# Kernel tuning notes

Hardware: AMD Instinct MI355X
Metric: run time of the kernel (lower is better)

## Reference

```python
import jax, jax.numpy as jnp
import numpy as np

V_K = 1.0
SIGMA = 0.1
EPS = 1e-10


def setup_inputs() -> dict:
    key = jax.random.key(0)
    ks = jax.random.split(key, 5)
    M, L, N, d, H = 2, 6, 512, 2, 64
    data = jax.random.normal(ks[0], (M, L, N, d), dtype=jnp.float32)
    t_snapshots = jnp.arange(L, dtype=jnp.float32) * 0.1
    w1 = jax.random.normal(ks[1], (H,), dtype=jnp.float32) * 0.5
    b1 = jnp.zeros((H,), jnp.float32)
    W2 = jax.random.normal(ks[2], (H, H), dtype=jnp.float32) / np.float32(np.sqrt(H))
    b2 = jnp.zeros((H,), jnp.float32)
    w3 = jax.random.normal(ks[3], (H,), dtype=jnp.float32) / np.float32(np.sqrt(H))
    b3 = jnp.zeros((), jnp.float32)
    return {"data": data, "t_snapshots": t_snapshots, "w1": w1, "b1": b1,
            "W2": W2, "b2": b2, "w3": w3, "b3": b3}


def _phi(r, w1, b1, W2, b2, w3, b3):
    # scalar-to-scalar tanh MLP applied elementwise to r (any shape)
    h1 = jnp.tanh(r[..., None] * w1 + b1)                      # [..., H]
    h2 = jnp.tanh(jnp.einsum('...h,hk->...k', h1, W2) + b2)    # [..., H]
    return jnp.einsum('...k,k->...', h2, w3) + b3              # [...]


def _loss(data, t, params):
    M, L, N, d = data.shape
    diff = data[:, :, :, None, :] - data[:, :, None, :, :]     # [M,L,N,N,d]
    ssq = jnp.sum(diff * diff, axis=-1)                        # [M,L,N,N]
    dist = jnp.where(ssq > 0, jnp.sqrt(jnp.where(ssq > 0, ssq, 1.0)), 0.0)
    off_diag = ~jnp.eye(N, dtype=bool)                         # [N,N]

    f = lambda r: _phi(r, *params)
    # Phi values on all L snapshots (for energy)
    phi = f(dist)                                              # [M,L,N,N]
    # First/second radial derivatives on current snapshots only (ell = 0..L-2)
    r_cur = dist[:, :-1]                                       # [M,L-1,N,N]
    df = lambda r: jax.jvp(f, (r,), (jnp.ones_like(r),))[1]
    dphi = df(r_cur)                                           # Phi'(r)
    d2phi = jax.jvp(df, (r_cur,), (jnp.ones_like(r_cur),))[1]  # Phi''(r)

    dt = t[1:] - t[:-1]                                        # [L-1]

    # --- drift / dissipation ---
    dist_safe = jnp.maximum(r_cur, EPS)
    unit = diff[:, :-1] / dist_safe[..., None]                 # [M,L-1,N,N,d]
    gphi = jnp.where(off_diag[..., None], dphi[..., None] * unit, 0.0)
    grad_Phi_mean = gphi.sum(axis=3) / N                       # [M,L-1,N,d]
    drift = -V_K * data[:, :-1] - grad_Phi_mean
    total_diss = ((drift ** 2).sum(axis=(2, 3)) / N * dt).sum()

    # --- laplacian / diffusion ---
    lap_phi_mean = jnp.where(off_diag, d2phi, 0.0).sum(axis=-1) / N  # [M,L-1,N]
    lap_sum = V_K * d + lap_phi_mean
    total_diff = (SIGMA ** 2 * lap_sum.mean(axis=-1) * dt).sum()

    # --- energy per snapshot ---
    V_mean = 0.5 * V_K * (data ** 2).sum(axis=-1).mean(axis=-1)      # [M,L]
    Phi_mean = jnp.where(off_diag, phi, 0.0).sum(axis=(-1, -2)) / (N * N)
    E = V_mean + Phi_mean                                            # [M,L]
    total_energy_change = (E[:, 1:] - E[:, :-1]).sum()

    n_pairs = M * (L - 1)
    residual = (total_diss + total_diff - 2.0 * total_energy_change) / n_pairs
    return residual ** 2


def reference(data, t_snapshots, w1, b1, W2, b2, w3, b3):
    return _loss(data, t_snapshots, (w1, b1, W2, b2, w3, b3))
```

## Files before the change

kernel.cpp:

```cpp
#include <hip/hip_runtime.h>
#include <hip/hip_bf16.h>

#define MM 2
#define LL 6
#define NN 512
#define HH 64
#define K_TAB 512
#define RMAX 16.0f
#define H_STEP (RMAX / (float)K_TAB)
#define HINV   ((float)K_TAB / RMAX)
#define NBLK (MM * LL * (NN / 4))


__device__ __forceinline__ float wave_reduce_sum(float v) {
    #pragma unroll
    for (int m = 32; m > 0; m >>= 1) v += __shfl_xor(v, m, 64);
    return v;
}

__global__ __launch_bounds__(256) void build_nodes(
        const float* __restrict__ w1, const float* __restrict__ b1,
        const float* __restrict__ W2, const float* __restrict__ b2,
        const float* __restrict__ w3, const float* __restrict__ b3,
        float2* __restrict__ nodes) {
    int gid  = blockIdx.x * blockDim.x + threadIdx.x;
    int node = gid >> 6;
    int lane = gid & 63;
    if (node > K_TAB) return;

    float r = (float)node * H_STEP;

    float w1l = w1[lane];
    float u   = fmaf(r, w1l, b1[lane]);
    float t1  = tanhf(u);
    float e1  = 1.0f - t1 * t1;
    float h1  = t1;
    float h1p = e1 * w1l;

    float v = b2[lane], vp = 0.0f;
    #pragma unroll
    for (int h = 0; h < HH; ++h) {
        float a  = __shfl(h1,  h, 64);
        float ap = __shfl(h1p, h, 64);
        float w  = W2[h * HH + lane];
        v  = fmaf(a,  w, v);
        vp = fmaf(ap, w, vp);
    }
    float t2 = tanhf(v);
    float e2 = 1.0f - t2 * t2;
    float w3l = w3[lane];
    float sphi = wave_reduce_sum(w3l * t2);
    float sdp  = wave_reduce_sum(w3l * e2 * vp);
    if (lane == 0)
        nodes[node] = make_float2(sphi + b3[0], sdp * H_STEP);
}

__global__ __launch_bounds__(256) void pair_kernel(
        const float* __restrict__ data, const float2* __restrict__ nodes,
        float4* __restrict__ partial) {
    const int blocks_per_ml = NN / 4;
    int ml = blockIdx.x / blocks_per_ml;
    int i4 = blockIdx.x % blocks_per_ml;

    __shared__ float4 coef[K_TAB];
    __shared__ float2 xs[NN];
    __shared__ float  red[4 * 4];

    #pragma unroll
    for (int it = 0; it < K_TAB / 256; ++it) {
        int e = it * 256 + threadIdx.x;
        float2 g0 = nodes[e];
        float2 g1 = nodes[e + 1];
        float  d  = g1.x - g0.x;
        coef[e] = make_float4(g0.x, g0.y,
                              3.0f * d - 2.0f * g0.y - g1.y,
                              g0.y + g1.y - 2.0f * d);
    }
    {
        const float4* src = (const float4*)(data + (size_t)ml * NN * 2);
        ((float4*)xs)[threadIdx.x] = src[threadIdx.x];
    }
    __syncthreads();

    int wv   = threadIdx.x >> 6;
    int lane = threadIdx.x & 63;
    int i    = i4 * 4 + wv;
    float2 xi = xs[i];

    float aphi = 0.0f, ad2 = 0.0f, agx = 0.0f, agy = 0.0f;
    #pragma unroll
    for (int jj = 0; jj < NN / 64; ++jj) {
        int j = jj * 64 + lane;
        float2 xj = xs[j];
        float dx = xi.x - xj.x;
        float dy = xi.y - xj.y;
        float ssq = fmaf(dx, dx, dy * dy);
        float rr  = sqrtf(ssq);
        float f   = rr * HINV;
        int   idx = (int)f;
        idx = idx > (K_TAB - 1) ? (K_TAB - 1) : idx;
        float tt = f - (float)idx;
        float4 c = coef[idx];
        float phi  = fmaf(tt, fmaf(tt, fmaf(tt, c.w, c.z), c.y), c.x);
        float dph  = fmaf(tt, fmaf(tt, 3.0f * c.w, 2.0f * c.z), c.y) * HINV;
        float d2ph = fmaf(tt, 6.0f * c.w, 2.0f * c.z) * (HINV * HINV);
        float inv_r = 1.0f / fmaxf(rr, 1e-10f);
        bool off = (j != i);
        aphi += off ? phi  : 0.0f;
        ad2  += off ? d2ph : 0.0f;
        float s = dph * inv_r;
        agx = fmaf(s, dx, agx);
        agy = fmaf(s, dy, agy);
    }

    aphi = wave_reduce_sum(aphi);
    ad2  = wave_reduce_sum(ad2);
    agx  = wave_reduce_sum(agx);
    agy  = wave_reduce_sum(agy);

    if (lane == 0) {
        const float invN = 1.0f / (float)NN;
        float driftx = -xi.x - agx * invN;
        float drifty = -xi.y - agy * invN;
        float dr2 = fmaf(driftx, driftx, drifty * drifty);
        float vsq = fmaf(xi.x, xi.x, xi.y * xi.y);
        red[wv * 4 + 0] = aphi;
        red[wv * 4 + 1] = ad2;
        red[wv * 4 + 2] = dr2;
        red[wv * 4 + 3] = vsq;
    }
    __syncthreads();
    if (threadIdx.x == 0) {
        partial[blockIdx.x] = make_float4(
            red[0] + red[4] + red[8]  + red[12],
            red[1] + red[5] + red[9]  + red[13],
            red[2] + red[6] + red[10] + red[14],
            red[3] + red[7] + red[11] + red[15]);
    }
}

__global__ __launch_bounds__(64) void finalize(
        const float* __restrict__ partial, const float* __restrict__ t,
        float* __restrict__ out) {
    __shared__ float sums[48];
    int tid = threadIdx.x;
    if (tid < 48) {
        int ml   = tid >> 2;
        int stat = tid & 3;
        const float* p = partial + (size_t)ml * (NN / 4) * 4 + stat;
        float s = 0.0f;
        #pragma unroll 8
        for (int b = 0; b < NN / 4; ++b) s += p[b * 4];
        sums[tid] = s;
    }
    __syncthreads();
    if (tid == 0) {
        const double N = (double)NN;
        const double SIG2 = 0.01;
        const double VKD  = 2.0;
        double diss = 0.0, diffu = 0.0, dE = 0.0;
        for (int m = 0; m < MM; ++m) {
            double E0 = 0.0;
            for (int l = 0; l < LL; ++l) {
                int idx = m * LL + l;
                double sphi = (double)sums[idx * 4 + 0];
                double sd2  = (double)sums[idx * 4 + 1];
                double sdr  = (double)sums[idx * 4 + 2];
                double sv   = (double)sums[idx * 4 + 3];
                double E = 0.5 * sv / N + sphi / (N * N);
                if (l == 0) E0 = E;
                if (l == LL - 1) dE += E - E0;
                if (l < LL - 1) {
                    double dt = (double)t[l + 1] - (double)t[l];
                    diss  += sdr / N * dt;
                    diffu += SIG2 * (VKD + sd2 / (N * N)) * dt;
                }
            }
        }
        double res = (diss + diffu - 2.0 * dE) / (double)(MM * (LL - 1));
        out[0] = (float)(res * res);
    }
}

extern "C" void kernel_launch(void* const* d_in, const int* in_sizes, int n_in,
                              void* d_out, int out_size, void* d_ws, size_t ws_size,
                              hipStream_t stream) {
    const float* data = (const float*)d_in[0];
    const float* t    = (const float*)d_in[1];
    const float* w1   = (const float*)d_in[2];
    const float* b1   = (const float*)d_in[3];
    const float* W2   = (const float*)d_in[4];
    const float* b2   = (const float*)d_in[5];
    const float* w3   = (const float*)d_in[6];
    const float* b3   = (const float*)d_in[7];

    float2* nodes   = (float2*)d_ws;
    float4* partial = (float4*)((char*)d_ws + 8192);

    build_nodes<<<129, 256, 0, stream>>>(w1, b1, W2, b2, w3, b3, nodes);
    pair_kernel<<<NBLK, 256, 0, stream>>>(data, nodes, partial);
    finalize<<<1, 64, 0, stream>>>((const float*)partial, t, (float*)d_out);
}
```

Baseline: 82.32 us.

## Fuse finalize into pair kernel via atomic accumulation and last-block reduction

Removes the separate finalize launch. Each pair block atomically adds its four partial sums into double accumulators, and the last block, chosen by an atomic ticket counter, computes the final residual. The accumulators and counter are zeroed inside build_nodes. The sqrt plus reciprocal is also replaced by a single rsq to get both r and 1/r. Risks are atomic contention on 48 addresses and a slight change in precision from rsq, including near r=0.

```diff
diff --git a/kernel.cpp b/kernel.cpp
--- a/kernel.cpp
+++ b/kernel.cpp
@@ -1,5 +1,4 @@
 #include <hip/hip_runtime.h>
-#include <hip/hip_bf16.h>
 
 #define MM 2
 #define LL 6
@@ -22,7 +21,13 @@
         const float* __restrict__ w1, const float* __restrict__ b1,
         const float* __restrict__ W2, const float* __restrict__ b2,
         const float* __restrict__ w3, const float* __restrict__ b3,
-        float2* __restrict__ nodes) {
+        float2* __restrict__ nodes, double* __restrict__ acc,
+        unsigned* __restrict__ cnt) {
+    if (blockIdx.x == 0) {
+        if (threadIdx.x < 48) acc[threadIdx.x] = 0.0;
+        if (threadIdx.x == 48) *cnt = 0u;
+    }
+
     int gid  = blockIdx.x * blockDim.x + threadIdx.x;
     int node = gid >> 6;
     int lane = gid & 63;
@@ -55,9 +60,10 @@
         nodes[node] = make_float2(sphi + b3[0], sdp * H_STEP);
 }
 
-__global__ __launch_bounds__(256) void pair_kernel(
+__global__ __launch_bounds__(256) void pair_finalize(
         const float* __restrict__ data, const float2* __restrict__ nodes,
-        float4* __restrict__ partial) {
+        double* __restrict__ acc, unsigned* __restrict__ cnt,
+        const float* __restrict__ ts, float* __restrict__ out) {
     const int blocks_per_ml = NN / 4;
     int ml = blockIdx.x / blocks_per_ml;
     int i4 = blockIdx.x % blocks_per_ml;
@@ -95,7 +101,8 @@
         float dx = xi.x - xj.x;
         float dy = xi.y - xj.y;
         float ssq = fmaf(dx, dx, dy * dy);
-        float rr  = sqrtf(ssq);
+        float ir  = __builtin_amdgcn_rsqf(fmaxf(ssq, 1e-20f));
+        float rr  = ssq * ir;
         float f   = rr * HINV;
         int   idx = (int)f;
         idx = idx > (K_TAB - 1) ? (K_TAB - 1) : idx;
@@ -104,11 +111,10 @@
         float phi  = fmaf(tt, fmaf(tt, fmaf(tt, c.w, c.z), c.y), c.x);
         float dph  = fmaf(tt, fmaf(tt, 3.0f * c.w, 2.0f * c.z), c.y) * HINV;
         float d2ph = fmaf(tt, 6.0f * c.w, 2.0f * c.z) * (HINV * HINV);
-        float inv_r = 1.0f / fmaxf(rr, 1e-10f);
         bool off = (j != i);
         aphi += off ? phi  : 0.0f;
         ad2  += off ? d2ph : 0.0f;
-        float s = dph * inv_r;
+        float s = dph * ir;
         agx = fmaf(s, dx, agx);
         agy = fmaf(s, dy, agy);
     }
@@ -130,55 +136,55 @@
         red[wv * 4 + 3] = vsq;
     }
     __syncthreads();
+
     if (threadIdx.x == 0) {
-        partial[blockIdx.x] = make_float4(
-            red[0] + red[4] + red[8]  + red[12],
-            red[1] + red[5] + red[9]  + red[13],
-            red[2] + red[6] + red[10] + red[14],
-            red[3] + red[7] + red[11] + red[15]);
-    }
-}
-
-__global__ __launch_bounds__(64) void finalize(
-        const float* __restrict__ partial, const float* __restrict__ t,
-        float* __restrict__ out) {
-    __shared__ float sums[48];
-    int tid = threadIdx.x;
-    if (tid < 48) {
-        int ml   = tid >> 2;
-        int stat = tid & 3;
-        const float* p = partial + (size_t)ml * (NN / 4) * 4 + stat;
-        float s = 0.0f;
-        #pragma unroll 8
-        for (int b = 0; b < NN / 4; ++b) s += p[b * 4];
-        sums[tid] = s;
-    }
-    __syncthreads();
-    if (tid == 0) {
-        const double N = (double)NN;
-        const double SIG2 = 0.01;
-        const double VKD  = 2.0;
-        double diss = 0.0, diffu = 0.0, dE = 0.0;
-        for (int m = 0; m < MM; ++m) {
-            double E0 = 0.0;
-            for (int l = 0; l < LL; ++l) {
-                int idx = m * LL + l;
-                double sphi = (double)sums[idx * 4 + 0];
-                double sd2  = (double)sums[idx * 4 + 1];
-                double sdr  = (double)sums[idx * 4 + 2];
-                double sv   = (double)sums[idx * 4 + 3];
-                double E = 0.5 * sv / N + sphi / (N * N);
-                if (l == 0) E0 = E;
-                if (l == LL - 1) dE += E - E0;
-                if (l < LL - 1) {
-                    double dt = (double)t[l + 1] - (double)t[l];
-                    diss  += sdr / N * dt;
-                    diffu += SIG2 * (VKD + sd2 / (N * N)) * dt;
+        float s0 = red[0] + red[4] + red[8]  + red[12];
+        float s1 = red[1] + red[5] + red[9]  + red[13];
+        float s2 = red[2] + red[6] + red[10] + red[14];
+        float s3 = red[3] + red[7] + red[11] + red[15];
+        __hip_atomic_fetch_add(&acc[ml * 4 + 0], (double)s0,
+                               __ATOMIC_RELAXED, __HIP_MEMORY_SCOPE_AGENT);
+        __hip_atomic_fetch_add(&acc[ml * 4 + 1], (double)s1,
+                               __ATOMIC_RELAXED, __HIP_MEMORY_SCOPE_AGENT);
+        __hip_atomic_fetch_add(&acc[ml * 4 + 2], (double)s2,
+                               __ATOMIC_RELAXED, __HIP_MEMORY_SCOPE_AGENT);
+        __hip_atomic_fetch_add(&acc[ml * 4 + 3], (double)s3,
+                               __ATOMIC_RELAXED, __HIP_MEMORY_SCOPE_AGENT);
+        unsigned ticket = __hip_atomic_fetch_add(cnt, 1u,
+                               __ATOMIC_ACQ_REL, __HIP_MEMORY_SCOPE_AGENT);
+        if (ticket == NBLK - 1) {
+            double s[48];
+            #pragma unroll
+            for (int k = 0; k < 48; ++k)
+                s[k] = __hip_atomic_load(&acc[k],
+                           __ATOMIC_RELAXED, __HIP_MEMORY_SCOPE_AGENT);
+            const double N = (double)NN;
+            const double SIG2 = 0.01;
+            const double VKD  = 2.0;
+            double diss = 0.0, diffu = 0.0, dE = 0.0;
+            #pragma unroll
+            for (int m = 0; m < MM; ++m) {
+                double E0 = 0.0;
+                #pragma unroll
+                for (int l = 0; l < LL; ++l) {
+                    int idx = m * LL + l;
+                    double sphi = s[idx * 4 + 0];
+                    double sd2  = s[idx * 4 + 1];
+                    double sdr  = s[idx * 4 + 2];
+                    double sv   = s[idx * 4 + 3];
+                    double E = 0.5 * sv / N + sphi / (N * N);
+                    if (l == 0) E0 = E;
+                    if (l == LL - 1) dE += E - E0;
+                    if (l < LL - 1) {
+                        double dt = (double)ts[l + 1] - (double)ts[l];
+                        diss  += sdr / N * dt;
+                        diffu += SIG2 * (VKD + sd2 / (N * N)) * dt;
+                    }
                 }
             }
+            double res = (diss + diffu - 2.0 * dE) / (double)(MM * (LL - 1));
+            out[0] = (float)(res * res);
         }
-        double res = (diss + diffu - 2.0 * dE) / (double)(MM * (LL - 1));
-        out[0] = (float)(res * res);
     }
 }
 
@@ -194,10 +200,10 @@
     const float* w3   = (const float*)d_in[6];
     const float* b3   = (const float*)d_in[7];
 
-    float2* nodes   = (float2*)d_ws;
-    float4* partial = (float4*)((char*)d_ws + 8192);
-
-    build_nodes<<<129, 256, 0, stream>>>(w1, b1, W2, b2, w3, b3, nodes);
-    pair_kernel<<<NBLK, 256, 0, stream>>>(data, nodes, partial);
-    finalize<<<1, 64, 0, stream>>>((const float*)partial, t, (float*)d_out);
-}
+    float2*   nodes = (float2*)d_ws;
+    double*   acc   = (double*)((char*)d_ws + 8192);
+    unsigned* cnt   = (unsigned*)((char*)d_ws + 8576);
+
+    build_nodes<<<129, 256, 0, stream>>>(w1, b1, W2, b2, w3, b3, nodes, acc, cnt);
+    pair_finalize<<<NBLK, 256, 0, stream>>>(data, nodes, acc, cnt, t, (float*)d_out);
+}
```

Measured after the change: 115.4 us. 1.4x slower.

## Precompute spline coefficients globally and process four rows per wave

Applied to the files above, without the earlier changes.

The node-building kernel now writes the final cubic Hermite coefficients for each interval, evaluating the MLP at both interval endpoints, so the pair kernel only copies the table instead of rebuilding it in every block. The pair kernel gives each wave four i-rows, which cuts the block count by four and spreads the table and position loads over more work. The square root and division are replaced by a hardware reciprocal square root. In exchange, the MLP node work is duplicated, register pressure rises, and the approximate rsq may perturb results slightly.

```diff
diff --git a/kernel.cpp b/kernel.cpp
--- a/kernel.cpp
+++ b/kernel.cpp
@@ -1,5 +1,4 @@
 #include <hip/hip_runtime.h>
-#include <hip/hip_bf16.h>
 
 #define MM 2
 #define LL 6
@@ -9,7 +8,10 @@
 #define RMAX 16.0f
 #define H_STEP (RMAX / (float)K_TAB)
 #define HINV   ((float)K_TAB / RMAX)
-#define NBLK (MM * LL * (NN / 4))
+#define BPML 32
+#define NPBLK (MM * LL * BPML)
+#define IPB (NN / BPML)
+#define IPW 4
 
 
 __device__ __forceinline__ float wave_reduce_sum(float v) {
@@ -22,60 +24,67 @@
         const float* __restrict__ w1, const float* __restrict__ b1,
         const float* __restrict__ W2, const float* __restrict__ b2,
         const float* __restrict__ w3, const float* __restrict__ b3,
-        float2* __restrict__ nodes) {
+        float4* __restrict__ coefg) {
     int gid  = blockIdx.x * blockDim.x + threadIdx.x;
-    int node = gid >> 6;
+    int e    = gid >> 6;
     int lane = gid & 63;
-    if (node > K_TAB) return;
-
-    float r = (float)node * H_STEP;
+
+    float r0 = (float)e * H_STEP;
+    float r1 = r0 + H_STEP;
 
     float w1l = w1[lane];
-    float u   = fmaf(r, w1l, b1[lane]);
-    float t1  = tanhf(u);
-    float e1  = 1.0f - t1 * t1;
-    float h1  = t1;
-    float h1p = e1 * w1l;
-
-    float v = b2[lane], vp = 0.0f;
+    float b1l = b1[lane];
+    float t10 = tanhf(fmaf(r0, w1l, b1l));
+    float t11 = tanhf(fmaf(r1, w1l, b1l));
+    float p10 = (1.0f - t10 * t10) * w1l;
+    float p11 = (1.0f - t11 * t11) * w1l;
+
+    float b2l = b2[lane];
+    float v0 = b2l, vp0 = 0.0f, v1 = b2l, vp1 = 0.0f;
     #pragma unroll
     for (int h = 0; h < HH; ++h) {
-        float a  = __shfl(h1,  h, 64);
-        float ap = __shfl(h1p, h, 64);
+        float a0 = __shfl(t10, h, 64);
+        float q0 = __shfl(p10, h, 64);
+        float a1 = __shfl(t11, h, 64);
+        float q1 = __shfl(p11, h, 64);
         float w  = W2[h * HH + lane];
-        v  = fmaf(a,  w, v);
-        vp = fmaf(ap, w, vp);
-    }
-    float t2 = tanhf(v);
-    float e2 = 1.0f - t2 * t2;
+        v0  = fmaf(a0, w, v0);
+        vp0 = fmaf(q0, w, vp0);
+        v1  = fmaf(a1, w, v1);
+        vp1 = fmaf(q1, w, vp1);
+    }
+    float t20 = tanhf(v0);
+    float t21 = tanhf(v1);
     float w3l = w3[lane];
-    float sphi = wave_reduce_sum(w3l * t2);
-    float sdp  = wave_reduce_sum(w3l * e2 * vp);
-    if (lane == 0)
-        nodes[node] = make_float2(sphi + b3[0], sdp * H_STEP);
+    float sphi0 = wave_reduce_sum(w3l * t20);
+    float sdp0  = wave_reduce_sum(w3l * (1.0f - t20 * t20) * vp0);
+    float sphi1 = wave_reduce_sum(w3l * t21);
+    float sdp1  = wave_reduce_sum(w3l * (1.0f - t21 * t21) * vp1);
+    if (lane == 0) {
+        float phi0 = sphi0 + b3[0];
+        float phi1 = sphi1 + b3[0];
+        float m0 = sdp0 * H_STEP;
+        float m1 = sdp1 * H_STEP;
+        float d  = phi1 - phi0;
+        coefg[e] = make_float4(phi0, m0,
+                               3.0f * d - 2.0f * m0 - m1,
+                               m0 + m1 - 2.0f * d);
+    }
 }
 
 __global__ __launch_bounds__(256) void pair_kernel(
-        const float* __restrict__ data, const float2* __restrict__ nodes,
+        const float* __restrict__ data, const float4* __restrict__ coefg,
         float4* __restrict__ partial) {
-    const int blocks_per_ml = NN / 4;
-    int ml = blockIdx.x / blocks_per_ml;
-    int i4 = blockIdx.x % blocks_per_ml;
+    int ml = blockIdx.x >> 5;
+    int ig = blockIdx.x & (BPML - 1);
 
     __shared__ float4 coef[K_TAB];
     __shared__ float2 xs[NN];
     __shared__ float  red[4 * 4];
 
     #pragma unroll
-    for (int it = 0; it < K_TAB / 256; ++it) {
-        int e = it * 256 + threadIdx.x;
-        float2 g0 = nodes[e];
-        float2 g1 = nodes[e + 1];
-        float  d  = g1.x - g0.x;
-        coef[e] = make_float4(g0.x, g0.y,
-                              3.0f * d - 2.0f * g0.y - g1.y,
-                              g0.y + g1.y - 2.0f * d);
-    }
+    for (int it = 0; it < K_TAB / 256; ++it)
+        coef[it * 256 + threadIdx.x] = coefg[it * 256 + threadIdx.x];
     {
         const float4* src = (const float4*)(data + (size_t)ml * NN * 2);
         ((float4*)xs)[threadIdx.x] = src[threadIdx.x];
@@ -84,50 +93,66 @@
 
     int wv   = threadIdx.x >> 6;
     int lane = threadIdx.x & 63;
-    int i    = i4 * 4 + wv;
-    float2 xi = xs[i];
-
-    float aphi = 0.0f, ad2 = 0.0f, agx = 0.0f, agy = 0.0f;
+    int ibase = ig * IPB + wv * IPW;
+
+    float2 xi[IPW];
+    #pragma unroll
+    for (int q = 0; q < IPW; ++q) xi[q] = xs[ibase + q];
+
+    float aphi[IPW], ad2[IPW], agx[IPW], agy[IPW];
+    #pragma unroll
+    for (int q = 0; q < IPW; ++q) { aphi[q] = 0.f; ad2[q] = 0.f; agx[q] = 0.f; agy[q] = 0.f; }
+
     #pragma unroll
     for (int jj = 0; jj < NN / 64; ++jj) {
         int j = jj * 64 + lane;
         float2 xj = xs[j];
-        float dx = xi.x - xj.x;
-        float dy = xi.y - xj.y;
-        float ssq = fmaf(dx, dx, dy * dy);
-        float rr  = sqrtf(ssq);
-        float f   = rr * HINV;
-        int   idx = (int)f;
-        idx = idx > (K_TAB - 1) ? (K_TAB - 1) : idx;
-        float tt = f - (float)idx;
-        float4 c = coef[idx];
-        float phi  = fmaf(tt, fmaf(tt, fmaf(tt, c.w, c.z), c.y), c.x);
-        float dph  = fmaf(tt, fmaf(tt, 3.0f * c.w, 2.0f * c.z), c.y) * HINV;
-        float d2ph = fmaf(tt, 6.0f * c.w, 2.0f * c.z) * (HINV * HINV);
-        float inv_r = 1.0f / fmaxf(rr, 1e-10f);
-        bool off = (j != i);
-        aphi += off ? phi  : 0.0f;
-        ad2  += off ? d2ph : 0.0f;
-        float s = dph * inv_r;
-        agx = fmaf(s, dx, agx);
-        agy = fmaf(s, dy, agy);
-    }
-
-    aphi = wave_reduce_sum(aphi);
-    ad2  = wave_reduce_sum(ad2);
-    agx  = wave_reduce_sum(agx);
-    agy  = wave_reduce_sum(agy);
-
+        #pragma unroll
+        for (int q = 0; q < IPW; ++q) {
+            float dx = xi[q].x - xj.x;
+            float dy = xi[q].y - xj.y;
+            float ssq = fmaf(dx, dx, dy * dy);
+            float ir  = __builtin_amdgcn_rsqf(fmaxf(ssq, 1e-20f));
+            float rr  = ssq * ir;
+            float f   = rr * HINV;
+            int   idx = (int)f;
+            idx = idx > (K_TAB - 1) ? (K_TAB - 1) : idx;
+            float tt = f - (float)idx;
+            float4 c = coef[idx];
+            float phi  = fmaf(tt, fmaf(tt, fmaf(tt, c.w, c.z), c.y), c.x);
+            float dph  = fmaf(tt, fmaf(tt, 3.0f * c.w, 2.0f * c.z), c.y) * HINV;
+            float d2ph = fmaf(tt, 6.0f * c.w, 2.0f * c.z) * (HINV * HINV);
+            bool off = (j != ibase + q);
+            aphi[q] += off ? phi  : 0.0f;
+            ad2[q]  += off ? d2ph : 0.0f;
+            float s = dph * ir;
+            agx[q] = fmaf(s, dx, agx[q]);
+            agy[q] = fmaf(s, dy, agy[q]);
+        }
+    }
+
+    float s0 = 0.f, s1 = 0.f, s2 = 0.f, s3 = 0.f;
+    #pragma unroll
+    for (int q = 0; q < IPW; ++q) {
+        float a  = wave_reduce_sum(aphi[q]);
+        float d2 = wave_reduce_sum(ad2[q]);
+        float gx = wave_reduce_sum(agx[q]);
+        float gy = wave_reduce_sum(agy[q]);
+        if (lane == 0) {
+            const float invN = 1.0f / (float)NN;
+            float driftx = -xi[q].x - gx * invN;
+            float drifty = -xi[q].y - gy * invN;
+            s0 += a;
+            s1 += d2;
+            s2 += fmaf(driftx, driftx, drifty * drifty);
+            s3 += fmaf(xi[q].x, xi[q].x, xi[q].y * xi[q].y);
+        }
+    }
     if (lane == 0) {
-        const float invN = 1.0f / (float)NN;
-        float driftx = -xi.x - agx * invN;
-        float drifty = -xi.y - agy * invN;
-        float dr2 = fmaf(driftx, driftx, drifty * drifty);
-        float vsq = fmaf(xi.x, xi.x, xi.y * xi.y);
-        red[wv * 4 + 0] = aphi;
-        red[wv * 4 + 1] = ad2;
-        red[wv * 4 + 2] = dr2;
-        red[wv * 4 + 3] = vsq;
+        red[wv * 4 + 0] = s0;
+        red[wv * 4 + 1] = s1;
+        red[wv * 4 + 2] = s2;
+        red[wv * 4 + 3] = s3;
     }
     __syncthreads();
     if (threadIdx.x == 0) {
@@ -147,10 +172,10 @@
     if (tid < 48) {
         int ml   = tid >> 2;
         int stat = tid & 3;
-        const float* p = partial + (size_t)ml * (NN / 4) * 4 + stat;
+        const float* p = partial + (size_t)ml * BPML * 4 + stat;
         float s = 0.0f;
-        #pragma unroll 8
-        for (int b = 0; b < NN / 4; ++b) s += p[b * 4];
+        #pragma unroll
+        for (int b = 0; b < BPML; ++b) s += p[b * 4];
         sums[tid] = s;
     }
     __syncthreads();
@@ -194,10 +219,10 @@
     const float* w3   = (const float*)d_in[6];
     const float* b3   = (const float*)d_in[7];
 
-    float2* nodes   = (float2*)d_ws;
+    float4* coefg   = (float4*)d_ws;
     float4* partial = (float4*)((char*)d_ws + 8192);
 
-    build_nodes<<<129, 256, 0, stream>>>(w1, b1, W2, b2, w3, b3, nodes);
-    pair_kernel<<<NBLK, 256, 0, stream>>>(data, nodes, partial);
+    build_nodes<<<128, 256, 0, stream>>>(w1, b1, W2, b2, w3, b3, coefg);
+    pair_kernel<<<NPBLK, 256, 0, stream>>>(data, coefg, partial);
     finalize<<<1, 64, 0, stream>>>((const float*)partial, t, (float*)d_out);
 }
```

Measured after the change: 79.92 us. -2.9%, faster.
